# Performance work log

Hardware: AMD Instinct MI355X
Metric: run time of the kernel (lower is better)

Reference implementation:

```python
import jax, jax.numpy as jnp
import numpy as np

NEG = -1e6  # mask fill value used by d2l.sequence_mask


def setup_inputs() -> dict:
    key = jax.random.key(0)
    k1, k2, k3, k4, k5, k6, k7 = jax.random.split(key, 7)
    B, Q, K, DQ, DK, H, DV = 8, 256, 1024, 256, 256, 128, 128
    queries = jax.random.normal(k1, (B, Q, DQ), dtype=jnp.float32)
    keys = jax.random.normal(k2, (B, K, DK), dtype=jnp.float32)
    values = jax.random.normal(k3, (B, K, DV), dtype=jnp.float32)
    valid_lens = jax.random.randint(k4, (B,), 1, K + 1, dtype=jnp.int32)
    # learned params (nn.Linear stores weight as [out, in]; apply as x @ W.T)
    W_q = jax.random.normal(k5, (H, DQ), dtype=jnp.float32) / np.sqrt(DQ)
    W_k = jax.random.normal(k6, (H, DK), dtype=jnp.float32) / np.sqrt(DK)
    w_v = jax.random.normal(k7, (H,), dtype=jnp.float32) / np.sqrt(H)
    return {"queries": queries, "keys": keys, "values": values,
            "valid_lens": valid_lens, "W_q": W_q, "W_k": W_k, "w_v": w_v}


def reference(queries, keys, values, valid_lens, W_q, W_k, w_v):
    # projections
    q = jnp.einsum('bqd,hd->bqh', queries, W_q)   # [B,Q,H]
    k = jnp.einsum('bkd,hd->bkh', keys, W_k)      # [B,K,H]
    # broadcast add + tanh -> [B,Q,K,H] (the fusion-headroom intermediate)
    features = jnp.tanh(q[:, :, None, :] + k[:, None, :, :])
    scores = jnp.einsum('bqkh,h->bqk', features, w_v)  # [B,Q,K]
    # masked softmax: valid_lens is per-batch (dim==1 path)
    klen = scores.shape[-1]
    mask = jnp.arange(klen)[None, None, :] < valid_lens[:, None, None]
    scores = jnp.where(mask, scores, NEG)
    weights = jax.nn.softmax(scores, axis=-1)
    # dropout is identity in eval mode
    return jnp.einsum('bqk,bkv->bqv', weights, values)
```

## Files before the change

### kernel.cpp

```cpp
#include <hip/hip_runtime.h>


#define Bb 8
#define Qn 256
#define Kk 1024
#define Dd 256
#define Hh 128
#define DVv 128

__device__ __forceinline__ float fexp2(float x) { return __builtin_amdgcn_exp2f(x); }
__device__ __forceinline__ float frcp(float x)  { return __builtin_amdgcn_rcpf(x); }

__global__ __launch_bounds__(256)
void repack_w(const float* __restrict__ Wq, const float* __restrict__ Wk,
              float4* __restrict__ Wq4T, float4* __restrict__ Wk4T)
{
    const int blk = blockIdx.x;
    const float* src = (blk < 32) ? Wq : Wk;
    float4*      dst = (blk < 32) ? Wq4T : Wk4T;
    const int idx = (blk & 31) * 256 + threadIdx.x;
    const int g = idx >> 7;
    const int h = idx & 127;
    dst[idx] = *(const float4*)(src + (size_t)h * Dd + g * 4);
}

__global__ __launch_bounds__(512)
void proj_exp_kernel(const float* __restrict__ queries,
                     const float* __restrict__ keys,
                     const float4* __restrict__ Wq4T,
                     const float4* __restrict__ Wk4T,
                     float* __restrict__ EqT,
                     float* __restrict__ EkT)
{
    __shared__ __align__(16) float Xs[16 * 256];
    const int blk = blockIdx.x;
    const float* X; const float4* W4; float* outT; int RB; int i0;
    if (blk < 128) { X = queries; W4 = Wq4T; outT = EqT; RB = Qn; i0 = blk * 16; }
    else           { X = keys;    W4 = Wk4T; outT = EkT; RB = Kk; i0 = (blk - 128) * 16; }
    const int tid = threadIdx.x;
    const int h   = tid & 127;
    const int r4  = __builtin_amdgcn_readfirstlane(tid >> 7);

    {
        const float4* xsrc = (const float4*)(X + (size_t)i0 * Dd);
#pragma unroll
        for (int s = 0; s < 2; ++s) {
            const int idx = tid + 512 * s;
            *(float4*)(Xs + idx * 4) = xsrc[idx];
        }
    }
    __syncthreads();

    float acc[4] = {0.f, 0.f, 0.f, 0.f};
    const float4* wp = W4 + h;
    const float*  xr = Xs + (r4 * 4) * 256;
#pragma unroll 8
    for (int g = 0; g < 64; ++g) {
        const float4 w = wp[(size_t)g * 128];
#pragma unroll
        for (int i = 0; i < 4; ++i) {
            const float4 x = *(const float4*)(xr + i * 256 + g * 4);
            acc[i] = fmaf(x.x, w.x, acc[i]);
            acc[i] = fmaf(x.y, w.y, acc[i]);
            acc[i] = fmaf(x.z, w.z, acc[i]);
            acc[i] = fmaf(x.w, w.w, acc[i]);
        }
    }
    const int b    = i0 / RB;
    const int rloc = (i0 % RB) + r4 * 4;
    float4 o;
    o.x = fexp2(acc[0] * 2.885390082f);
    o.y = fexp2(acc[1] * 2.885390082f);
    o.z = fexp2(acc[2] * 2.885390082f);
    o.w = fexp2(acc[3] * 2.885390082f);
    *(float4*)(outT + (size_t)b * Hh * RB + (size_t)h * RB + rloc) = o;
}

__global__ __launch_bounds__(256)
void score_kernel(const float* __restrict__ EqT,
                  const float* __restrict__ EkT,
                  const float* __restrict__ wv,
                  const int* __restrict__ valid_lens,
                  float* __restrict__ S)
{
    __shared__ __align__(16) float eqs[128 * 8];
    __shared__ __align__(16) float w2s[128];
    const int blk = blockIdx.x;
    const int b   = blk & 7;
    const int rem = blk >> 3;
    const int kt  = rem & 3;
    const int qt  = rem >> 2;
    const int len = valid_lens[b];
    if (kt * 256 >= len) return;

    const int tid = threadIdx.x;
    const int k   = kt * 256 + tid;
    const int q0  = qt * 8;

    {
        const int hh = tid >> 1, part = tid & 1;
        *(float4*)(eqs + hh * 8 + part * 4) =
            *(const float4*)(EqT + (size_t)b * Hh * Qn + (size_t)hh * Qn + q0 + part * 4);
        if (tid < 128) w2s[tid] = -2.0f * wv[tid];
    }
    __syncthreads();

    if ((k & ~63) >= len) return;

    const float* ekp = EkT + (size_t)b * Hh * Kk + k;
    float a[8];
#pragma unroll
    for (int j = 0; j < 8; ++j) a[j] = 0.f;

#pragma unroll 2
    for (int hg = 0; hg < 32; ++hg) {
        const int h = hg << 2;
        const float ek0 = ekp[(size_t)(h + 0) * Kk];
        const float ek1 = ekp[(size_t)(h + 1) * Kk];
        const float ek2 = ekp[(size_t)(h + 2) * Kk];
        const float ek3 = ekp[(size_t)(h + 3) * Kk];
        const float4 w = *(const float4*)(w2s + h);
        float eq[4][8];
#pragma unroll
        for (int i = 0; i < 4; ++i) {
            *(float4*)(&eq[i][0]) = *(const float4*)(eqs + (h + i) * 8);
            *(float4*)(&eq[i][4]) = *(const float4*)(eqs + (h + i) * 8 + 4);
        }
#pragma unroll
        for (int j = 0; j < 8; ++j) {
            const float A  = fmaf(eq[0][j], ek0, 1.0f);
            const float B  = fmaf(eq[1][j], ek1, 1.0f);
            const float C  = fmaf(eq[2][j], ek2, 1.0f);
            const float E  = fmaf(eq[3][j], ek3, 1.0f);
            const float AB = A * B;
            const float CE = C * E;
            const float N1 = fmaf(w.x, B, w.y * A);
            const float N2 = fmaf(w.z, E, w.w * C);
            const float N  = fmaf(N1, CE, N2 * AB);
            a[j] = fmaf(N, frcp(AB * CE), a[j]);
        }
    }
    float* srow = S + (size_t)(b * Qn + q0) * Kk + k;
#pragma unroll
    for (int j = 0; j < 8; ++j) srow[(size_t)j * Kk] = a[j];
}

__global__ __launch_bounds__(512)
void softmax_pv_kernel(const float* __restrict__ S,
                       const float* __restrict__ values,
                       const int* __restrict__ valid_lens,
                       float* __restrict__ out)
{
    __shared__ float  s_sc[4][Kk];
    __shared__ float4 s_part[7][4][32];
    __shared__ float  s_inv[4];

    const int blk  = blockIdx.x;
    const int b    = blk & 7;
    const int q0   = (blk >> 3) << 2;
    const int tid  = threadIdx.x;
    const int lane = tid & 63;
    const int wave = __builtin_amdgcn_readfirstlane(tid >> 6);
    const int len  = valid_lens[b];

#pragma unroll
    for (int j = 0; j < 4; ++j) {
        const float* sr = S + (size_t)(b * Qn + q0 + j) * Kk;
        for (int k = tid; k < len; k += 512) s_sc[j][k] = sr[k];
    }
    __syncthreads();

    if (wave < 4) {
        const int q = wave;
        float m = -3.0e38f;
        for (int i = lane; i < len; i += 64) m = fmaxf(m, s_sc[q][i]);
#pragma unroll
        for (int off = 32; off > 0; off >>= 1) m = fmaxf(m, __shfl_xor(m, off));
        float sum = 0.f;
        for (int i = lane; i < len; i += 64) {
            const float p = fexp2((s_sc[q][i] - m) * 1.44269504f);
            s_sc[q][i] = p;
            sum += p;
        }
#pragma unroll
        for (int off = 32; off > 0; off >>= 1) sum += __shfl_xor(sum, off);
        if (lane == 0) s_inv[q] = frcp(sum);
    }
    __syncthreads();

    {
        const int slice = tid >> 5;
        const int l32   = tid & 31;
        const int v4    = l32 << 2;
        const float* vp = values + (size_t)b * Kk * DVv + v4;
        float a[4][4];
#pragma unroll
        for (int q = 0; q < 4; ++q) { a[q][0]=0.f; a[q][1]=0.f; a[q][2]=0.f; a[q][3]=0.f; }
        for (int k = slice; k < len; k += 16) {
            const float4 val = *(const float4*)(vp + (size_t)k * DVv);
            const float w0 = s_sc[0][k], w1 = s_sc[1][k], w2 = s_sc[2][k], w3 = s_sc[3][k];
            a[0][0] = fmaf(w0, val.x, a[0][0]);
            a[0][1] = fmaf(w0, val.y, a[0][1]);
            a[0][2] = fmaf(w0, val.z, a[0][2]);
            a[0][3] = fmaf(w0, val.w, a[0][3]);
            a[1][0] = fmaf(w1, val.x, a[1][0]);
            a[1][1] = fmaf(w1, val.y, a[1][1]);
            a[1][2] = fmaf(w1, val.z, a[1][2]);
            a[1][3] = fmaf(w1, val.w, a[1][3]);
            a[2][0] = fmaf(w2, val.x, a[2][0]);
            a[2][1] = fmaf(w2, val.y, a[2][1]);
            a[2][2] = fmaf(w2, val.z, a[2][2]);
            a[2][3] = fmaf(w2, val.w, a[2][3]);
            a[3][0] = fmaf(w3, val.x, a[3][0]);
            a[3][1] = fmaf(w3, val.y, a[3][1]);
            a[3][2] = fmaf(w3, val.z, a[3][2]);
            a[3][3] = fmaf(w3, val.w, a[3][3]);
        }
#pragma unroll
        for (int q = 0; q < 4; ++q)
#pragma unroll
            for (int x = 0; x < 4; ++x) a[q][x] += __shfl_xor(a[q][x], 32);
        if (wave > 0 && lane < 32) {
#pragma unroll
            for (int q = 0; q < 4; ++q)
                s_part[wave - 1][q][l32] = make_float4(a[q][0], a[q][1], a[q][2], a[q][3]);
        }
        __syncthreads();
        if (wave == 0 && lane < 32) {
#pragma unroll
            for (int q = 0; q < 4; ++q) {
                float r0 = a[q][0], r1 = a[q][1], r2 = a[q][2], r3 = a[q][3];
#pragma unroll
                for (int w = 0; w < 7; ++w) {
                    const float4 p = s_part[w][q][l32];
                    r0 += p.x; r1 += p.y; r2 += p.z; r3 += p.w;
                }
                const float inv = s_inv[q];
                *(float4*)(out + (size_t)(b * Qn + q0 + q) * DVv + v4) =
                    make_float4(r0 * inv, r1 * inv, r2 * inv, r3 * inv);
            }
        }
    }
}

extern "C" void kernel_launch(void* const* d_in, const int* in_sizes, int n_in,
                              void* d_out, int out_size, void* d_ws, size_t ws_size,
                              hipStream_t stream) {
    (void)in_sizes; (void)n_in; (void)out_size; (void)ws_size;
    const float* queries    = (const float*)d_in[0];
    const float* keys       = (const float*)d_in[1];
    const float* values     = (const float*)d_in[2];
    const int*   valid_lens = (const int*)  d_in[3];
    const float* Wq         = (const float*)d_in[4];
    const float* Wk         = (const float*)d_in[5];
    const float* wvv        = (const float*)d_in[6];
    float* out = (float*)d_out;

    float* Wq4T = (float*)d_ws;
    float* Wk4T = Wq4T + (size_t)Dd * Hh;
    float* EqT  = Wk4T + (size_t)Dd * Hh;
    float* EkT  = EqT + (size_t)Bb * Hh * Qn;
    float* S    = EkT + (size_t)Bb * Hh * Kk;

    repack_w       <<<  64, 256, 0, stream>>>(Wq, Wk, (float4*)Wq4T, (float4*)Wk4T);
    proj_exp_kernel<<< 640, 512, 0, stream>>>(queries, keys, (const float4*)Wq4T,
                                              (const float4*)Wk4T, EqT, EkT);
    score_kernel   <<<1024, 256, 0, stream>>>(EqT, EkT, wvv, valid_lens, S);
    softmax_pv_kernel<<<512, 512, 0, stream>>>(S, values, valid_lens, out);
}
```

Before: 139.5 us.

## Fuse score computation into softmax-PV kernel, drop global score buffer

Merges the score kernel into the softmax/PV kernel, so each 512-thread block computes scores for 4 queries across all keys directly into shared memory. This removes the global write and re-read of the B×Q×K score matrix and one kernel launch. In exchange each thread now handles 4 queries instead of 8, so every EkT load is reused for half as many score evaluations and total EkT traffic doubles. There are half as many score blocks. The partial-sum buffer is aliased onto the score shared memory behind an extra barrier.

```diff
diff --git a/kernel.cpp b/kernel.cpp
--- a/kernel.cpp
+++ b/kernel.cpp
@@ -76,97 +76,92 @@
     *(float4*)(outT + (size_t)b * Hh * RB + (size_t)h * RB + rloc) = o;
 }
 
-__global__ __launch_bounds__(256)
-void score_kernel(const float* __restrict__ EqT,
-                  const float* __restrict__ EkT,
-                  const float* __restrict__ wv,
-                  const int* __restrict__ valid_lens,
-                  float* __restrict__ S)
+__global__ __launch_bounds__(512)
+void score_softmax_pv_kernel(const float* __restrict__ EqT,
+                             const float* __restrict__ EkT,
+                             const float* __restrict__ wv,
+                             const int* __restrict__ valid_lens,
+                             const float* __restrict__ values,
+                             float* __restrict__ out)
 {
-    __shared__ __align__(16) float eqs[128 * 8];
-    __shared__ __align__(16) float w2s[128];
-    const int blk = blockIdx.x;
-    const int b   = blk & 7;
-    const int rem = blk >> 3;
-    const int kt  = rem & 3;
-    const int qt  = rem >> 2;
-    const int len = valid_lens[b];
-    if (kt * 256 >= len) return;
-
-    const int tid = threadIdx.x;
-    const int k   = kt * 256 + tid;
-    const int q0  = qt * 8;
-
-    {
-        const int hh = tid >> 1, part = tid & 1;
-        *(float4*)(eqs + hh * 8 + part * 4) =
-            *(const float4*)(EqT + (size_t)b * Hh * Qn + (size_t)hh * Qn + q0 + part * 4);
-        if (tid < 128) w2s[tid] = -2.0f * wv[tid];
-    }
-    __syncthreads();
-
-    if ((k & ~63) >= len) return;
-
-    const float* ekp = EkT + (size_t)b * Hh * Kk + k;
-    float a[8];
-#pragma unroll
-    for (int j = 0; j < 8; ++j) a[j] = 0.f;
-
-#pragma unroll 2
-    for (int hg = 0; hg < 32; ++hg) {
-        const int h = hg << 2;
-        const float ek0 = ekp[(size_t)(h + 0) * Kk];
-        const float ek1 = ekp[(size_t)(h + 1) * Kk];
-        const float ek2 = ekp[(size_t)(h + 2) * Kk];
-        const float ek3 = ekp[(size_t)(h + 3) * Kk];
-        const float4 w = *(const float4*)(w2s + h);
-        float eq[4][8];
-#pragma unroll
-        for (int i = 0; i < 4; ++i) {
-            *(float4*)(&eq[i][0]) = *(const float4*)(eqs + (h + i) * 8);
-            *(float4*)(&eq[i][4]) = *(const float4*)(eqs + (h + i) * 8 + 4);
-        }
-#pragma unroll
-        for (int j = 0; j < 8; ++j) {
-            const float A  = fmaf(eq[0][j], ek0, 1.0f);
-            const float B  = fmaf(eq[1][j], ek1, 1.0f);
-            const float C  = fmaf(eq[2][j], ek2, 1.0f);
-            const float E  = fmaf(eq[3][j], ek3, 1.0f);
-            const float AB = A * B;
-            const float CE = C * E;
-            const float N1 = fmaf(w.x, B, w.y * A);
-            const float N2 = fmaf(w.z, E, w.w * C);
-            const float N  = fmaf(N1, CE, N2 * AB);
-            a[j] = fmaf(N, frcp(AB * CE), a[j]);
-        }
-    }
-    float* srow = S + (size_t)(b * Qn + q0) * Kk + k;
-#pragma unroll
-    for (int j = 0; j < 8; ++j) srow[(size_t)j * Kk] = a[j];
-}
-
-__global__ __launch_bounds__(512)
-void softmax_pv_kernel(const float* __restrict__ S,
-                       const float* __restrict__ values,
-                       const int* __restrict__ valid_lens,
-                       float* __restrict__ out)
-{
-    __shared__ float  s_sc[4][Kk];
-    __shared__ float4 s_part[7][4][32];
-    __shared__ float  s_inv[4];
+    __shared__ __align__(16) float s_sc[4][Kk];
+    __shared__ __align__(16) float eqs[Hh * 4];
+    __shared__ __align__(16) float w2s[Hh];
+    __shared__ float s_inv[4];
 
     const int blk  = blockIdx.x;
     const int b    = blk & 7;
-    const int q0   = (blk >> 3) << 2;
+    const int qt   = blk >> 3;
+    const int q0   = qt * 4;
+    const int len  = valid_lens[b];
     const int tid  = threadIdx.x;
     const int lane = tid & 63;
     const int wave = __builtin_amdgcn_readfirstlane(tid >> 6);
-    const int len  = valid_lens[b];
-
-#pragma unroll
-    for (int j = 0; j < 4; ++j) {
-        const float* sr = S + (size_t)(b * Qn + q0 + j) * Kk;
-        for (int k = tid; k < len; k += 512) s_sc[j][k] = sr[k];
+
+    if (tid < 128) {
+        *(float4*)(eqs + tid * 4) =
+            *(const float4*)(EqT + (size_t)b * Hh * Qn + (size_t)tid * Qn + q0);
+    } else if (tid < 256) {
+        w2s[tid - 128] = -2.0f * wv[tid - 128];
+    }
+    __syncthreads();
+
+    const float* ekbase = EkT + (size_t)b * Hh * Kk;
+#pragma unroll
+    for (int kk = 0; kk < 2; ++kk) {
+        const int k = tid + kk * 512;
+        if ((k & ~63) >= len) continue;
+        const float* ekp = ekbase + k;
+        float a0 = 0.f, a1 = 0.f, a2 = 0.f, a3 = 0.f;
+#pragma unroll 2
+        for (int hg = 0; hg < 32; ++hg) {
+            const int h = hg << 2;
+            const float ek0 = ekp[(size_t)(h + 0) * Kk];
+            const float ek1 = ekp[(size_t)(h + 1) * Kk];
+            const float ek2 = ekp[(size_t)(h + 2) * Kk];
+            const float ek3 = ekp[(size_t)(h + 3) * Kk];
+            const float4 w  = *(const float4*)(w2s + h);
+            const float4 e0 = *(const float4*)(eqs + (h + 0) * 4);
+            const float4 e1 = *(const float4*)(eqs + (h + 1) * 4);
+            const float4 e2 = *(const float4*)(eqs + (h + 2) * 4);
+            const float4 e3 = *(const float4*)(eqs + (h + 3) * 4);
+            {
+                const float A = fmaf(e0.x, ek0, 1.0f), B = fmaf(e1.x, ek1, 1.0f);
+                const float C = fmaf(e2.x, ek2, 1.0f), E = fmaf(e3.x, ek3, 1.0f);
+                const float AB = A * B, CE = C * E;
+                const float N = fmaf(fmaf(w.x, B, w.y * A), CE,
+                                     fmaf(w.z, E, w.w * C) * AB);
+                a0 = fmaf(N, frcp(AB * CE), a0);
+            }
+            {
+                const float A = fmaf(e0.y, ek0, 1.0f), B = fmaf(e1.y, ek1, 1.0f);
+                const float C = fmaf(e2.y, ek2, 1.0f), E = fmaf(e3.y, ek3, 1.0f);
+                const float AB = A * B, CE = C * E;
+                const float N = fmaf(fmaf(w.x, B, w.y * A), CE,
+                                     fmaf(w.z, E, w.w * C) * AB);
+                a1 = fmaf(N, frcp(AB * CE), a1);
+            }
+            {
+                const float A = fmaf(e0.z, ek0, 1.0f), B = fmaf(e1.z, ek1, 1.0f);
+                const float C = fmaf(e2.z, ek2, 1.0f), E = fmaf(e3.z, ek3, 1.0f);
+                const float AB = A * B, CE = C * E;
+                const float N = fmaf(fmaf(w.x, B, w.y * A), CE,
+                                     fmaf(w.z, E, w.w * C) * AB);
+                a2 = fmaf(N, frcp(AB * CE), a2);
+            }
+            {
+                const float A = fmaf(e0.w, ek0, 1.0f), B = fmaf(e1.w, ek1, 1.0f);
+                const float C = fmaf(e2.w, ek2, 1.0f), E = fmaf(e3.w, ek3, 1.0f);
+                const float AB = A * B, CE = C * E;
+                const float N = fmaf(fmaf(w.x, B, w.y * A), CE,
+                                     fmaf(w.z, E, w.w * C) * AB);
+                a3 = fmaf(N, frcp(AB * CE), a3);
+            }
+        }
+        s_sc[0][k] = a0;
+        s_sc[1][k] = a1;
+        s_sc[2][k] = a2;
+        s_sc[3][k] = a3;
     }
     __syncthreads();
 
@@ -220,6 +215,9 @@
         for (int q = 0; q < 4; ++q)
 #pragma unroll
             for (int x = 0; x < 4; ++x) a[q][x] += __shfl_xor(a[q][x], 32);
+
+        __syncthreads();
+        float4 (*s_part)[4][32] = (float4 (*)[4][32])(&s_sc[0][0]);
         if (wave > 0 && lane < 32) {
 #pragma unroll
             for (int q = 0; q < 4; ++q)
@@ -260,11 +258,10 @@
     float* Wk4T = Wq4T + (size_t)Dd * Hh;
     float* EqT  = Wk4T + (size_t)Dd * Hh;
     float* EkT  = EqT + (size_t)Bb * Hh * Qn;
-    float* S    = EkT + (size_t)Bb * Hh * Kk;
 
     repack_w       <<<  64, 256, 0, stream>>>(Wq, Wk, (float4*)Wq4T, (float4*)Wk4T);
     proj_exp_kernel<<< 640, 512, 0, stream>>>(queries, keys, (const float4*)Wq4T,
                                               (const float4*)Wk4T, EqT, EkT);
-    score_kernel   <<<1024, 256, 0, stream>>>(EqT, EkT, wvv, valid_lens, S);
-    softmax_pv_kernel<<<512, 512, 0, stream>>>(S, values, valid_lens, out);
-}
+    score_softmax_pv_kernel<<<512, 512, 0, stream>>>(EqT, EkT, wvv, valid_lens,
+                                                     values, out);
+}
```

Result: faster. 133.5 us (-4.3%).
